# Kernel optimization log

Hardware: AMD Instinct MI355X
Metric: run time of the kernel (lower is better)

The kernel has to match this reference:

```python
import jax, jax.numpy as jnp
import numpy as np

B, S1, S2, D1, D2 = 4, 2048, 2048, 512, 512
H, DK, DV = 8, 64, 64


def setup_inputs() -> dict:
    key = jax.random.key(0)
    ks = jax.random.split(key, 8)
    x1 = jax.random.normal(ks[0], (B, S1, D1), dtype=jnp.float32)
    x2 = jax.random.normal(ks[1], (B, S2, D2), dtype=jnp.float32)
    x3 = jax.random.normal(ks[2], (B, S2, D2), dtype=jnp.float32)
    s = 0.02
    Wq = jax.random.normal(ks[3], (D1, H * DK), dtype=jnp.float32) * s
    Wk = jax.random.normal(ks[4], (D2, H * DK), dtype=jnp.float32) * s
    Wv = jax.random.normal(ks[5], (D2, H * DV), dtype=jnp.float32) * s
    Wo = jax.random.normal(ks[6], (H * DV, D1), dtype=jnp.float32) * s
    bo = jnp.zeros((D1,), dtype=jnp.float32)
    return {"x1": x1, "x2": x2, "x3": x3, "Wq": Wq, "Wk": Wk, "Wv": Wv, "Wo": Wo, "bo": bo}


def reference(x1, x2, x3, Wq, Wk, Wv, Wo, bo):
    b, s1, _ = x1.shape
    # project to per-head q, k, v: [B, H, S, Dh]
    q = (x1 @ Wq).reshape(b, s1, H, DK).transpose(0, 2, 1, 3)
    k = (x2 @ Wk).reshape(b, x2.shape[1], H, DK).transpose(0, 2, 1, 3)
    v = (x3 @ Wv).reshape(b, x3.shape[1], H, DV).transpose(0, 2, 1, 3)
    scores = jnp.einsum('bhqd,bhkd->bhqk', q, k) / jnp.sqrt(jnp.float32(DK))
    attn = jax.nn.softmax(scores, axis=-1)
    out = jnp.einsum('bhqk,bhkd->bhqd', attn, v)  # [B, H, S1, DV]
    out = out.transpose(0, 2, 1, 3).reshape(b, s1, H * DV)
    return out @ Wo + bo
```

## Files before the change

kernel.cpp:

```cpp
#include <hip/hip_runtime.h>

typedef __attribute__((ext_vector_type(4))) float f32x4;
typedef __attribute__((ext_vector_type(16))) float f32x16;
typedef __attribute__((ext_vector_type(8))) __bf16 bf16x8;
typedef __attribute__((ext_vector_type(4))) __bf16 bf16x4;
typedef __attribute__((ext_vector_type(2))) __bf16 bf16x2;
typedef __attribute__((ext_vector_type(4))) unsigned u32x4;

#define DEVINL __device__ __forceinline__

DEVINL void gld16(const void* g, void* l) {
  __builtin_amdgcn_global_load_lds((__attribute__((address_space(1))) void*)(void*)g,
                                   (__attribute__((address_space(3))) void*)l, 16, 0, 0);
}


__global__ __launch_bounds__(256) void cvt_all(const float* x1, const float* x2, const float* x3,
                                               const float* Wq, const float* Wk, const float* Wv,
                                               const float* Wo, __bf16* o0, __bf16* o1, __bf16* o2,
                                               __bf16* WT) {
  __shared__ float t[64][65];
  const int bx = blockIdx.x;
  if (bx < 12288) {
    const int z = bx >> 12;
    const float* s = z == 0 ? x1 : z == 1 ? x2 : x3;
    __bf16* d = z == 0 ? o0 : z == 1 ? o1 : o2;
    size_t i = (size_t)(bx & 4095) * 256 + threadIdx.x;
    f32x4 v = ((const f32x4*)s)[i];
    bf16x4 o;
#pragma unroll
    for (int j = 0; j < 4; ++j) o[j] = (__bf16)v[j];
    ((bf16x4*)d)[i] = o;
  } else {
    const int l = bx - 12288;
    const int z = l >> 6;
    const float* W = z == 0 ? Wq : z == 1 ? Wk : z == 2 ? Wv : Wo;
    __bf16* D = WT + (size_t)z * 512 * 512;
    const int r0 = ((l >> 3) & 7) * 64, c0 = (l & 7) * 64;
    const int tx = threadIdx.x & 63, ty = threadIdx.x >> 6;
#pragma unroll
    for (int j = 0; j < 16; ++j)
      t[ty + j * 4][tx] = W[(size_t)(r0 + ty + j * 4) * 512 + c0 + tx];
    __syncthreads();
#pragma unroll
    for (int j = 0; j < 16; ++j)
      D[(size_t)(c0 + ty + j * 4) * 512 + r0 + tx] = (__bf16)t[tx][ty + j * 4];
  }
}


DEVINL void gemm_tile(const __bf16* A, const __bf16* Bt, int m0, int n0,
                      __bf16* As, __bf16* Bs, f32x4 acc[4][4]) {
  const int tid = threadIdx.x, lane = tid & 63, w = tid >> 6;
  const int qd = lane >> 4, r = lane & 15;
  const int wm = w & 1, wn = w >> 1;
  const char* ap[4];
  const char* bp[4];
#pragma unroll
  for (int j = 0; j < 4; ++j) {
    int c = (w * 4 + j) * 64 + lane;
    int row = c >> 3, cs = c & 7;
    int gc = cs ^ (row & 7);
    ap[j] = (const char*)A + (size_t)(m0 + row) * 1024 + gc * 16;
    bp[j] = (const char*)Bt + (size_t)(n0 + row) * 1024 + gc * 16;
  }
  int offA[4][2], offB[4][2];
#pragma unroll
  for (int t = 0; t < 4; ++t)
#pragma unroll
    for (int ks = 0; ks < 2; ++ks) {
      int m = wm * 64 + t * 16 + r;
      offA[t][ks] = m * 128 + (((ks * 4 + qd) ^ (m & 7)) * 16);
      int n = wn * 64 + t * 16 + r;
      offB[t][ks] = n * 128 + (((ks * 4 + qd) ^ (n & 7)) * 16);
    }
  char* AsC = (char*)As;
  char* BsC = (char*)Bs;
  for (int kt = 0; kt < 8; ++kt) {
    __syncthreads();
#pragma unroll
    for (int j = 0; j < 4; ++j) {
      gld16(ap[j] + kt * 128, AsC + (w * 4 + j) * 1024);
      gld16(bp[j] + kt * 128, BsC + (w * 4 + j) * 1024);
    }
    __syncthreads();
#pragma unroll
    for (int ks = 0; ks < 2; ++ks) {
      bf16x8 a[4], b[4];
#pragma unroll
      for (int t = 0; t < 4; ++t) {
        a[t] = *(const bf16x8*)(AsC + offA[t][ks]);
        b[t] = *(const bf16x8*)(BsC + offB[t][ks]);
      }
#pragma unroll
      for (int i = 0; i < 4; ++i)
#pragma unroll
        for (int j2 = 0; j2 < 4; ++j2)
          acc[i][j2] = __builtin_amdgcn_mfma_f32_16x16x32_bf16(a[i], b[j2], acc[i][j2], 0, 0, 0);
    }
  }
}

__global__ __launch_bounds__(256, 3) void gemm_proj(const __bf16* x1b, const __bf16* x2b,
                                                    const __bf16* x3b, const __bf16* WT,
                                                    __bf16* Qo, __bf16* Ko, __bf16* Vto) {
  __shared__ __align__(16) char smem[34816];
  __bf16* As = (__bf16*)smem;
  __bf16* Bs = (__bf16*)(smem + 16384);
  const int z = blockIdx.z;
  const __bf16* A = z == 0 ? x1b : z == 1 ? x2b : x3b;
  const __bf16* Bt = WT + (size_t)z * 512 * 512;
  const int l = blockIdx.x;
  const int sidx = l >> 3;
  const int m0 = ((l & 7) * 8 + (sidx >> 2)) * 128;
  const int n0 = (sidx & 3) * 128;
  f32x4 acc[4][4] = {};
  gemm_tile(A, Bt, m0, n0, As, Bs, acc);
  const int tid = threadIdx.x, lane = tid & 63, w = tid >> 6;
  const int qd = lane >> 4, r = lane & 15, wm = w & 1, wn = w >> 1;
  const int b = m0 >> 11, sbase = m0 & 2047;
  if (z == 2) {
    __syncthreads();
    char* T = smem;
#pragma unroll
    for (int mt = 0; mt < 4; ++mt)
#pragma unroll
      for (int nt = 0; nt < 4; ++nt) {
        int dv = wn * 64 + nt * 16 + r;
        int sl = wm * 64 + mt * 16 + qd * 4;
        bf16x4 p4;
#pragma unroll
        for (int g = 0; g < 4; ++g) p4[g] = (__bf16)acc[mt][nt][g];
        *(bf16x4*)(T + (size_t)dv * 272 + sl * 2) = p4;
      }
    __syncthreads();
#pragma unroll
    for (int p2 = 0; p2 < 2; ++p2) {
      int dvrow = p2 * 64 + (tid >> 2);
      int col = n0 + dvrow, h = col >> 6, d = col & 63;
      __bf16* dst = Vto + ((size_t)(b * 8 + h) * 64 + d) * 2048 + sbase + (tid & 3) * 8;
#pragma unroll
      for (int j = 0; j < 4; ++j) {
        bf16x8 vv = *(const bf16x8*)(T + (size_t)dvrow * 272 + (tid & 3) * 16 + j * 64);
        *(bf16x8*)(dst + j * 32) = vv;
      }
    }
  } else {
    const float qscale = 0.18033688f;
#pragma unroll
    for (int mt = 0; mt < 4; ++mt) {
#pragma unroll
      for (int nt = 0; nt < 4; ++nt) {
        f32x4 v = acc[mt][nt];
        if (z == 0) {
#pragma unroll
          for (int g = 0; g < 4; ++g) v[g] *= qscale;
        }
        int col = n0 + wn * 64 + nt * 16 + r;
        int h = col >> 6, d = col & 63;
        int s = sbase + wm * 64 + mt * 16 + qd * 4;
        __bf16* O = (z == 0 ? Qo : Ko) + ((size_t)(b * 8 + h) * 2048 + s) * 64 + d;
#pragma unroll
        for (int g = 0; g < 4; ++g) O[(size_t)g * 64] = (__bf16)v[g];
      }
    }
  }
}

__global__ __launch_bounds__(256, 2) void gemm_out(const __bf16* Op, const float* Lp,
                                                   const __bf16* WoT, const float* bo,
                                                   float* out) {
  __shared__ __align__(16) __bf16 As[64 * 64];
  __shared__ __align__(16) __bf16 Bs[128 * 64];
  const int tid = threadIdx.x, lane = tid & 63, w = tid >> 6;
  const int qd = lane >> 4, r = lane & 15, wm = w & 1, wn = w >> 1;
  const int id = blockIdx.x;
  const int rest = id >> 3;
  const int m0 = ((id & 7) * 16 + (rest & 15)) * 64;
  const int n0 = (rest >> 4) * 128;
  const int b8 = (m0 >> 11) * 8;
  const int sb = m0 & 2047;
  const char* bp[4];
#pragma unroll
  for (int j = 0; j < 4; ++j) {
    int c = (w * 4 + j) * 64 + lane;
    int row = c >> 3, gc = (c & 7) ^ (row & 7);
    bp[j] = (const char*)WoT + (size_t)(n0 + row) * 1024 + gc * 16;
  }
  int arow[2], ach[2];
#pragma unroll
  for (int j = 0; j < 2; ++j) {
    int c = (w * 2 + j) * 64 + lane;
    arow[j] = c >> 3;
    ach[j] = c & 7;
  }
  int offA[2][2], offB[4][2];
#pragma unroll
  for (int ks = 0; ks < 2; ++ks) {
#pragma unroll
    for (int t = 0; t < 2; ++t) {
      int m = wm * 32 + t * 16 + r;
      offA[t][ks] = m * 128 + (((ks * 4 + qd) ^ (m & 7)) * 16);
    }
#pragma unroll
    for (int t = 0; t < 4; ++t) {
      int n = wn * 64 + t * 16 + r;
      offB[t][ks] = n * 128 + (((ks * 4 + qd) ^ (n & 7)) * 16);
    }
  }
  char* AsC = (char*)As;
  char* BsC = (char*)Bs;
  bf16x8 pa0[2], pa1[2];
  float pinv[2];
  auto loadA = [&](int h) {
#pragma unroll
    for (int j = 0; j < 2; ++j) {
      size_t rr = (size_t)(b8 + h) * 2048 + sb + arow[j];
      const __bf16* p0 = Op + rr * 64 + ach[j] * 8;
      pa0[j] = *(const bf16x8*)p0;
      pa1[j] = *(const bf16x8*)(p0 + (size_t)32 * 2048 * 64);
      pinv[j] = 1.0f / (Lp[rr] + Lp[rr + 65536]);
    }
  };
  loadA(0);
  f32x4 acc[2][4] = {};
  for (int kt = 0; kt < 8; ++kt) {
    __syncthreads();
#pragma unroll
    for (int j = 0; j < 4; ++j) gld16(bp[j] + kt * 128, BsC + (w * 4 + j) * 1024);
#pragma unroll
    for (int j = 0; j < 2; ++j) {
      bf16x8 q;
#pragma unroll
      for (int k2 = 0; k2 < 8; ++k2)
        q[k2] = (__bf16)(((float)pa0[j][k2] + (float)pa1[j][k2]) * pinv[j]);
      *(bf16x8*)(AsC + arow[j] * 128 + (ach[j] ^ (arow[j] & 7)) * 16) = q;
    }
    __syncthreads();
    if (kt < 7) loadA(kt + 1);
#pragma unroll
    for (int ks = 0; ks < 2; ++ks) {
      bf16x8 a[2], b[4];
#pragma unroll
      for (int t = 0; t < 2; ++t) a[t] = *(const bf16x8*)(AsC + offA[t][ks]);
#pragma unroll
      for (int t = 0; t < 4; ++t) b[t] = *(const bf16x8*)(BsC + offB[t][ks]);
#pragma unroll
      for (int i = 0; i < 2; ++i)
#pragma unroll
        for (int j2 = 0; j2 < 4; ++j2)
          acc[i][j2] = __builtin_amdgcn_mfma_f32_16x16x32_bf16(a[i], b[j2], acc[i][j2], 0, 0, 0);
    }
  }
#pragma unroll
  for (int nt = 0; nt < 4; ++nt) {
    int col = n0 + wn * 64 + nt * 16 + r;
    float bv = bo[col];
#pragma unroll
    for (int mt = 0; mt < 2; ++mt) {
      int mg = m0 + wm * 32 + mt * 16 + qd * 4;
#pragma unroll
      for (int g = 0; g < 4; ++g) out[(size_t)(mg + g) * 512 + col] = acc[mt][nt][g] + bv;
    }
  }
}

__global__ __launch_bounds__(256, 4) void attn(const __bf16* Q, const __bf16* K,
                                               const __bf16* Vt, __bf16* Opart, float* Lp) {
  __shared__ __align__(16) __bf16 Qs[128 * 64];
  __shared__ __align__(16) __bf16 Ksd[2][64 * 64];
  __shared__ __align__(16) __bf16 Vs[64 * 64];
  const int tid = threadIdx.x, lane = tid & 63, w = tid >> 6;
  const int l31 = lane & 31, lh = lane >> 5;
  const int id = blockIdx.x;
  const int rest = id >> 3;
  const int bh = (id & 7) * 4 + (rest >> 5);
  const int kvh = (rest >> 4) & 1;
  const int q0 = (rest & 15) * 128;
  const char* QgC = (const char*)(Q + ((size_t)bh * 2048 + q0) * 64);
  const char* KgC = (const char*)(K + (size_t)bh * 2048 * 64);
  const char* VgC = (const char*)(Vt + (size_t)bh * 64 * 2048);
  char* QsC = (char*)Qs;
  char* VsC = (char*)Vs;
  char* Kc = (char*)Ksd;
  char* Kn = (char*)Ksd + 8192;

  int koff[2], voff[2], ldso[2];
#pragma unroll
  for (int j = 0; j < 2; ++j) {
    int c = (w * 2 + j) * 64 + lane;
    int m = c >> 3, gc = (c & 7) ^ (m & 7);
    int ms = (m & ~12) | ((m & 4) << 1) | ((m & 8) >> 1);
    koff[j] = ms * 128 + gc * 16;
    voff[j] = m * 4096 + gc * 16;
    ldso[j] = (w * 2 + j) * 1024;
  }

  const int kt0 = kvh * 16;
  const size_t kb = (size_t)kt0 * 8192;
  const size_t vb = (size_t)kt0 * 128;

#pragma unroll
  for (int j = 0; j < 4; ++j) {
    int c = (w * 4 + j) * 64 + lane;
    int m = c >> 3, gc = (c & 7) ^ (m & 7);
    gld16(QgC + m * 128 + gc * 16, QsC + (w * 4 + j) * 1024);
  }
  gld16(KgC + kb + koff[0], Kc + ldso[0]);
  gld16(KgC + kb + koff[1], Kc + ldso[1]);
  gld16(VgC + vb + voff[0], VsC + ldso[0]);
  gld16(VgC + vb + voff[1], VsC + ldso[1]);
  gld16(KgC + kb + 8192 + koff[0], Kn + ldso[0]);
  gld16(KgC + kb + 8192 + koff[1], Kn + ldso[1]);
  __builtin_amdgcn_sched_barrier(0);
  asm volatile("s_waitcnt vmcnt(2)" ::: "memory");
  __builtin_amdgcn_sched_barrier(0);
  __builtin_amdgcn_s_barrier();
  __builtin_amdgcn_sched_barrier(0);

  const int rb = l31 * 128;
  const int he = (((lane & 7) ^ lh) << 4);
  const int qrow = (w * 32 + l31) * 128;

  bf16x8 ones;
#pragma unroll
  for (int j = 0; j < 8; ++j) ones[j] = (__bf16)1.0f;

  f32x16 oacc[2] = {};
  f32x16 lacc = {};
  bf16x8 pa[4];

  auto smhalf = [&](const f32x16& s, bf16x8& pa0, bf16x8& pa1) {
    unsigned wds[8];
#pragma unroll
    for (int i = 0; i < 8; ++i) {
      bf16x2 t;
      t[0] = (__bf16)__builtin_exp2f(s[2 * i]);
      t[1] = (__bf16)__builtin_exp2f(s[2 * i + 1]);
      wds[i] = __builtin_bit_cast(unsigned, t);
    }
    pa0 = __builtin_bit_cast(bf16x8, (u32x4){wds[0], wds[1], wds[2], wds[3]});
    pa1 = __builtin_bit_cast(bf16x8, (u32x4){wds[4], wds[5], wds[6], wds[7]});
  };
  auto qkchain = [&](const char* Kb, int half, const bf16x8 qf[4]) {
    f32x16 s = {};
#pragma unroll
    for (int c = 0; c < 4; ++c) {
      bf16x8 kf = *(const bf16x8*)(Kb + half * 4096 + rb + ((c << 5) ^ he));
      s = __builtin_amdgcn_mfma_f32_32x32x16_bf16(kf, qf[c], s, 0, 0, 0);
    }
    return s;
  };

  {
    bf16x8 qf[4];
#pragma unroll
    for (int c = 0; c < 4; ++c) qf[c] = *(const bf16x8*)(QsC + qrow + ((c << 5) ^ he));
    f32x16 s0 = qkchain(Kc, 0, qf);
    f32x16 s1 = qkchain(Kc, 1, qf);
    smhalf(s0, pa[0], pa[1]);
    smhalf(s1, pa[2], pa[3]);
  }
  __builtin_amdgcn_sched_barrier(0);
  asm volatile("s_waitcnt vmcnt(0)" ::: "memory");
  __builtin_amdgcn_sched_barrier(0);
  __builtin_amdgcn_s_barrier();
  __builtin_amdgcn_sched_barrier(0);

#pragma unroll 1
  for (int t = 0; t < 15; ++t) {
    __builtin_amdgcn_s_setprio(1);
#pragma unroll
    for (int c = 0; c < 4; ++c) {
      lacc = __builtin_amdgcn_mfma_f32_32x32x16_bf16(pa[c], ones, lacc, 0, 0, 0);
      bf16x8 vf0 = *(const bf16x8*)(VsC + rb + ((c << 5) ^ he));
      oacc[0] = __builtin_amdgcn_mfma_f32_32x32x16_bf16(pa[c], vf0, oacc[0], 0, 0, 0);
      bf16x8 vf1 = *(const bf16x8*)(VsC + 4096 + rb + ((c << 5) ^ he));
      oacc[1] = __builtin_amdgcn_mfma_f32_32x32x16_bf16(pa[c], vf1, oacc[1], 0, 0, 0);
    }
    bf16x8 qf[4];
#pragma unroll
    for (int c = 0; c < 4; ++c) qf[c] = *(const bf16x8*)(QsC + qrow + ((c << 5) ^ he));
    f32x16 s0 = qkchain(Kn, 0, qf);
    f32x16 s1 = qkchain(Kn, 1, qf);
    smhalf(s0, pa[0], pa[1]);
    __builtin_amdgcn_s_setprio(0);
    __builtin_amdgcn_sched_barrier(0);
    __builtin_amdgcn_s_barrier();
    __builtin_amdgcn_sched_barrier(0);

    gld16(VgC + vb + (size_t)(t + 1) * 128 + voff[0], VsC + ldso[0]);
    gld16(VgC + vb + (size_t)(t + 1) * 128 + voff[1], VsC + ldso[1]);
    if (t < 14) {
      gld16(KgC + kb + (size_t)(t + 2) * 8192 + koff[0], Kc + ldso[0]);
      gld16(KgC + kb + (size_t)(t + 2) * 8192 + koff[1], Kc + ldso[1]);
    }
    __builtin_amdgcn_sched_barrier(0);
    smhalf(s1, pa[2], pa[3]);
    __builtin_amdgcn_sched_barrier(0);
    asm volatile("s_waitcnt vmcnt(0)" ::: "memory");
    __builtin_amdgcn_sched_barrier(0);
    __builtin_amdgcn_s_barrier();
    __builtin_amdgcn_sched_barrier(0);

    char* tmp = Kc;
    Kc = Kn;
    Kn = tmp;
  }

#pragma unroll
  for (int c = 0; c < 4; ++c) {
    lacc = __builtin_amdgcn_mfma_f32_32x32x16_bf16(pa[c], ones, lacc, 0, 0, 0);
    bf16x8 vf0 = *(const bf16x8*)(VsC + rb + ((c << 5) ^ he));
    oacc[0] = __builtin_amdgcn_mfma_f32_32x32x16_bf16(pa[c], vf0, oacc[0], 0, 0, 0);
    bf16x8 vf1 = *(const bf16x8*)(VsC + 4096 + rb + ((c << 5) ^ he));
    oacc[1] = __builtin_amdgcn_mfma_f32_32x32x16_bf16(pa[c], vf1, oacc[1], 0, 0, 0);
  }

  const size_t pbase = (size_t)(kvh * 32 + bh) * 2048;
  if (l31 == 0) {
#pragma unroll
    for (int g = 0; g < 16; ++g)
      Lp[pbase + q0 + w * 32 + (g & 3) + 8 * (g >> 2) + 4 * lh] = lacc[g];
  }
  __bf16* Ob0 = Opart + pbase * 64;
#pragma unroll
  for (int dvt = 0; dvt < 2; ++dvt) {
#pragma unroll
    for (int g = 0; g < 16; ++g) {
      int s = q0 + w * 32 + (g & 3) + 8 * (g >> 2) + 4 * lh;
      Ob0[(size_t)s * 64 + dvt * 32 + l31] = (__bf16)oacc[dvt][g];
    }
  }
}


extern "C" void kernel_launch(void* const* d_in, const int* in_sizes, int n_in,
                              void* d_out, int out_size, void* d_ws, size_t ws_size,
                              hipStream_t stream) {
  const float* x1 = (const float*)d_in[0];
  const float* x2 = (const float*)d_in[1];
  const float* x3 = (const float*)d_in[2];
  const float* Wq = (const float*)d_in[3];
  const float* Wk = (const float*)d_in[4];
  const float* Wv = (const float*)d_in[5];
  const float* Wo = (const float*)d_in[6];
  const float* bo = (const float*)d_in[7];
  float* out = (float*)d_out;
  char* ws = (char*)d_ws;
  const size_t MB = 1ull << 20;
  __bf16* x1b = (__bf16*)(ws);
  __bf16* x2b = (__bf16*)(ws + 8 * MB);
  __bf16* x3b = (__bf16*)(ws + 16 * MB);
  __bf16* WT = (__bf16*)(ws + 24 * MB);
  __bf16* Qb = (__bf16*)(ws + 26 * MB);
  __bf16* Kb = (__bf16*)(ws + 34 * MB);
  __bf16* Vtb = (__bf16*)(ws + 42 * MB);
  __bf16* Opart = (__bf16*)(ws + 58 * MB);
  float* Lp = (float*)(ws + 74 * MB);

  cvt_all<<<dim3(12544), 256, 0, stream>>>(x1, x2, x3, Wq, Wk, Wv, Wo, x1b, x2b, x3b, WT);
  gemm_proj<<<dim3(256, 1, 3), 256, 0, stream>>>(x1b, x2b, x3b, WT, Qb, Kb, Vtb);
  attn<<<dim3(1024), 256, 0, stream>>>(Qb, Kb, Vtb, Opart, Lp);
  gemm_out<<<dim3(512), 256, 0, stream>>>(Opart, Lp, WT + 3ull * 512 * 512, bo, out);
}
```

Baseline: 188.8 us.

## Fuse fp32-to-bf16 activation conversion into projection GEMM A-tile loading

Removes the separate pass that converts x1/x2/x3 to bf16. The projection GEMM now reads the fp32 activations into registers, converts them and writes them swizzled into LDS, prefetching the next k-tile into registers. The goal is to avoid writing and re-reading 24MB of bf16 intermediates and to drop most of the conversion kernel. In exchange the GEMM's A operand costs more registers and gives up the async global_load_lds path, which could hurt occupancy or latency hiding.

```diff
diff --git a/kernel.cpp b/kernel.cpp
--- a/kernel.cpp
+++ b/kernel.cpp
@@ -15,54 +15,44 @@
 }
 
 
-__global__ __launch_bounds__(256) void cvt_all(const float* x1, const float* x2, const float* x3,
-                                               const float* Wq, const float* Wk, const float* Wv,
-                                               const float* Wo, __bf16* o0, __bf16* o1, __bf16* o2,
-                                               __bf16* WT) {
+__global__ __launch_bounds__(256) void cvt_w(const float* Wq, const float* Wk, const float* Wv,
+                                             const float* Wo, __bf16* WT) {
   __shared__ float t[64][65];
-  const int bx = blockIdx.x;
-  if (bx < 12288) {
-    const int z = bx >> 12;
-    const float* s = z == 0 ? x1 : z == 1 ? x2 : x3;
-    __bf16* d = z == 0 ? o0 : z == 1 ? o1 : o2;
-    size_t i = (size_t)(bx & 4095) * 256 + threadIdx.x;
-    f32x4 v = ((const f32x4*)s)[i];
-    bf16x4 o;
-#pragma unroll
-    for (int j = 0; j < 4; ++j) o[j] = (__bf16)v[j];
-    ((bf16x4*)d)[i] = o;
-  } else {
-    const int l = bx - 12288;
-    const int z = l >> 6;
-    const float* W = z == 0 ? Wq : z == 1 ? Wk : z == 2 ? Wv : Wo;
-    __bf16* D = WT + (size_t)z * 512 * 512;
-    const int r0 = ((l >> 3) & 7) * 64, c0 = (l & 7) * 64;
-    const int tx = threadIdx.x & 63, ty = threadIdx.x >> 6;
-#pragma unroll
-    for (int j = 0; j < 16; ++j)
-      t[ty + j * 4][tx] = W[(size_t)(r0 + ty + j * 4) * 512 + c0 + tx];
-    __syncthreads();
-#pragma unroll
-    for (int j = 0; j < 16; ++j)
-      D[(size_t)(c0 + ty + j * 4) * 512 + r0 + tx] = (__bf16)t[tx][ty + j * 4];
-  }
-}
-
-
-DEVINL void gemm_tile(const __bf16* A, const __bf16* Bt, int m0, int n0,
-                      __bf16* As, __bf16* Bs, f32x4 acc[4][4]) {
+  const int l = blockIdx.x;
+  const int z = l >> 6;
+  const float* W = z == 0 ? Wq : z == 1 ? Wk : z == 2 ? Wv : Wo;
+  __bf16* D = WT + (size_t)z * 512 * 512;
+  const int r0 = ((l >> 3) & 7) * 64, c0 = (l & 7) * 64;
+  const int tx = threadIdx.x & 63, ty = threadIdx.x >> 6;
+#pragma unroll
+  for (int j = 0; j < 16; ++j)
+    t[ty + j * 4][tx] = W[(size_t)(r0 + ty + j * 4) * 512 + c0 + tx];
+  __syncthreads();
+#pragma unroll
+  for (int j = 0; j < 16; ++j)
+    D[(size_t)(c0 + ty + j * 4) * 512 + r0 + tx] = (__bf16)t[tx][ty + j * 4];
+}
+
+
+DEVINL void gemm_tile_f32(const float* A, const __bf16* Bt, int m0, int n0,
+                          __bf16* As, __bf16* Bs, f32x4 acc[4][4]) {
   const int tid = threadIdx.x, lane = tid & 63, w = tid >> 6;
   const int qd = lane >> 4, r = lane & 15;
   const int wm = w & 1, wn = w >> 1;
-  const char* ap[4];
   const char* bp[4];
 #pragma unroll
   for (int j = 0; j < 4; ++j) {
     int c = (w * 4 + j) * 64 + lane;
-    int row = c >> 3, cs = c & 7;
-    int gc = cs ^ (row & 7);
-    ap[j] = (const char*)A + (size_t)(m0 + row) * 1024 + gc * 16;
+    int row = c >> 3, gc = (c & 7) ^ (row & 7);
     bp[j] = (const char*)Bt + (size_t)(n0 + row) * 1024 + gc * 16;
+  }
+  const int am = tid >> 4, ac = tid & 15;
+  const float* ap = A + (size_t)(m0 + am) * 512 + ac * 4;
+  int woff[8];
+#pragma unroll
+  for (int j = 0; j < 8; ++j) {
+    int m = j * 16 + am;
+    woff[j] = m * 128 + (((ac >> 1) ^ (m & 7)) << 4) + ((ac & 1) << 3);
   }
   int offA[4][2], offB[4][2];
 #pragma unroll
@@ -76,13 +66,25 @@
     }
   char* AsC = (char*)As;
   char* BsC = (char*)Bs;
+  f32x4 areg[8];
+  auto loadA = [&](int kt) {
+#pragma unroll
+    for (int j = 0; j < 8; ++j)
+      areg[j] = *(const f32x4*)(ap + (size_t)j * 16 * 512 + kt * 64);
+  };
+  loadA(0);
   for (int kt = 0; kt < 8; ++kt) {
     __syncthreads();
 #pragma unroll
-    for (int j = 0; j < 4; ++j) {
-      gld16(ap[j] + kt * 128, AsC + (w * 4 + j) * 1024);
-      gld16(bp[j] + kt * 128, BsC + (w * 4 + j) * 1024);
-    }
+    for (int j = 0; j < 8; ++j) {
+      bf16x4 o;
+#pragma unroll
+      for (int g = 0; g < 4; ++g) o[g] = (__bf16)areg[j][g];
+      *(bf16x4*)(AsC + woff[j]) = o;
+    }
+#pragma unroll
+    for (int j = 0; j < 4; ++j) gld16(bp[j] + kt * 128, BsC + (w * 4 + j) * 1024);
+    if (kt < 7) loadA(kt + 1);
     __syncthreads();
 #pragma unroll
     for (int ks = 0; ks < 2; ++ks) {
@@ -101,21 +103,21 @@
   }
 }
 
-__global__ __launch_bounds__(256, 3) void gemm_proj(const __bf16* x1b, const __bf16* x2b,
-                                                    const __bf16* x3b, const __bf16* WT,
+__global__ __launch_bounds__(256, 3) void gemm_proj(const float* x1, const float* x2,
+                                                    const float* x3, const __bf16* WT,
                                                     __bf16* Qo, __bf16* Ko, __bf16* Vto) {
   __shared__ __align__(16) char smem[34816];
   __bf16* As = (__bf16*)smem;
   __bf16* Bs = (__bf16*)(smem + 16384);
   const int z = blockIdx.z;
-  const __bf16* A = z == 0 ? x1b : z == 1 ? x2b : x3b;
+  const float* A = z == 0 ? x1 : z == 1 ? x2 : x3;
   const __bf16* Bt = WT + (size_t)z * 512 * 512;
   const int l = blockIdx.x;
   const int sidx = l >> 3;
   const int m0 = ((l & 7) * 8 + (sidx >> 2)) * 128;
   const int n0 = (sidx & 3) * 128;
   f32x4 acc[4][4] = {};
-  gemm_tile(A, Bt, m0, n0, As, Bs, acc);
+  gemm_tile_f32(A, Bt, m0, n0, As, Bs, acc);
   const int tid = threadIdx.x, lane = tid & 63, w = tid >> 6;
   const int qd = lane >> 4, r = lane & 15, wm = w & 1, wn = w >> 1;
   const int b = m0 >> 11, sbase = m0 & 2047;
@@ -449,9 +451,6 @@
   float* out = (float*)d_out;
   char* ws = (char*)d_ws;
   const size_t MB = 1ull << 20;
-  __bf16* x1b = (__bf16*)(ws);
-  __bf16* x2b = (__bf16*)(ws + 8 * MB);
-  __bf16* x3b = (__bf16*)(ws + 16 * MB);
   __bf16* WT = (__bf16*)(ws + 24 * MB);
   __bf16* Qb = (__bf16*)(ws + 26 * MB);
   __bf16* Kb = (__bf16*)(ws + 34 * MB);
@@ -459,8 +458,8 @@
   __bf16* Opart = (__bf16*)(ws + 58 * MB);
   float* Lp = (float*)(ws + 74 * MB);
 
-  cvt_all<<<dim3(12544), 256, 0, stream>>>(x1, x2, x3, Wq, Wk, Wv, Wo, x1b, x2b, x3b, WT);
-  gemm_proj<<<dim3(256, 1, 3), 256, 0, stream>>>(x1b, x2b, x3b, WT, Qb, Kb, Vtb);
+  cvt_w<<<dim3(256), 256, 0, stream>>>(Wq, Wk, Wv, Wo, WT);
+  gemm_proj<<<dim3(256, 1, 3), 256, 0, stream>>>(x1, x2, x3, WT, Qb, Kb, Vtb);
   attn<<<dim3(1024), 256, 0, stream>>>(Qb, Kb, Vtb, Opart, Lp);
   gemm_out<<<dim3(512), 256, 0, stream>>>(Opart, Lp, WT + 3ull * 512 * 512, bo, out);
 }
```

After: 184.7 us. -2.2%, faster.
